# Performance work log

Measured on AMD Instinct MI355X. Metric: run time of the kernel, lower is better.

## Reference

```python
import jax, jax.numpy as jnp
import numpy as np

B = 16384
NUM_DENSE = 13
NUM_SPARSE = 26
VOCAB = 100000
EMB = 64
MLP_DIMS = [512, 256, 64]
TOP_OUT = 256
TRIU_I, TRIU_J = np.triu_indices(NUM_SPARSE, k=1)  # 325 pairs


def setup_inputs() -> dict:
    key = jax.random.key(0)
    ks = jax.random.split(key, 12)
    inp = {}
    inp["dense_features"] = jax.random.normal(ks[0], (B, NUM_DENSE), dtype=jnp.float32)
    inp["sparse_features"] = jax.random.randint(ks[1], (B, NUM_SPARSE), 0, VOCAB, dtype=jnp.int64)
    # embedding tables, all same shape -> stacked [F, V, D]
    inp["tables"] = jax.random.normal(ks[2], (NUM_SPARSE, VOCAB, EMB), dtype=jnp.float32) * 0.01
    # bottom (dense) MLP: 13 -> 512 -> 256 -> 64, weights stored [in, out]
    dims = [NUM_DENSE] + MLP_DIMS
    for li in range(3):
        fan_in = dims[li]
        inp[f"W{li}"] = jax.random.normal(ks[3 + li], (dims[li], dims[li + 1]), dtype=jnp.float32) / np.sqrt(fan_in)
        inp[f"b{li}"] = jnp.zeros((dims[li + 1],), dtype=jnp.float32)
    # top MLP: (64 + 325) -> 256
    top_in = MLP_DIMS[-1] + NUM_SPARSE * (NUM_SPARSE - 1) // 2
    inp["Wt"] = jax.random.normal(ks[6], (top_in, TOP_OUT), dtype=jnp.float32) / np.sqrt(top_in)
    inp["bt"] = jnp.zeros((TOP_OUT,), dtype=jnp.float32)
    return inp


def reference(dense_features, sparse_features, tables, W0, b0, W1, b1, W2, b2, Wt, bt):
    # bottom MLP with ReLU after every layer (as in the torch Sequential)
    x = jax.nn.relu(dense_features @ W0 + b0)
    x = jax.nn.relu(x @ W1 + b1)
    dense_out = jax.nn.relu(x @ W2 + b2)  # [B, 64]

    # embedding gather: table f indexed by sparse_features[:, f] -> [B, F, D]
    emb = jax.vmap(lambda t, idx: t[idx], in_axes=(0, 1), out_axes=1)(tables, sparse_features)

    # pairwise dot interaction, upper triangle (i < j) -> [B, 325]
    gram = jnp.einsum('bid,bjd->bij', emb, emb)
    interact = gram[:, TRIU_I, TRIU_J]

    features = jnp.concatenate([dense_out, interact], axis=1)  # [B, 389]
    return features @ Wt + bt  # [B, 256]
```

## Files before the change

### kernel.cpp

```cpp
#include <hip/hip_runtime.h>
#include <hip/hip_bf16.h>


#define BATCH   16384
#define NSPARSE 26
#define VOCAB   100000
#define EMB     64
#define KTOP    416
#define KREAL   389
#define SPB     32
#define ASTR    424
#define X1STR   520
#define X2STR   264

typedef __attribute__((ext_vector_type(8)))  short bf16x8;
typedef __attribute__((ext_vector_type(4)))  short s16x4;
typedef __attribute__((ext_vector_type(4)))  float f32x4;
typedef __attribute__((ext_vector_type(16))) float f32x16;

__device__ inline void gload_lds16(const void* g, void* l) {
    __builtin_amdgcn_global_load_lds(
        (const __attribute__((address_space(1))) void*)g,
        (__attribute__((address_space(3))) void*)l, 16, 0, 0);
}

__device__ inline short f2bf(float x) {
    __hip_bfloat16 h = __float2bfloat16(x);
    return *reinterpret_cast<short*>(&h);
}

__global__ __launch_bounds__(256)
void prep_weights(const float* __restrict__ W0, const float* __restrict__ W1,
                  const float* __restrict__ W2, const float* __restrict__ Wt,
                  short* __restrict__ W0t, short* __restrict__ W1t,
                  short* __restrict__ W2t, short* __restrict__ Wtt)
{
    __shared__ float tile[32][36];
    int b = blockIdx.x, t = threadIdx.x;
    const float* src; short* dst; int K, N, Kpad, k0, n0;
    if (b < 16)        {              src = W0; dst = W0t; K = 13;  N = 512; Kpad = 32;  k0 = 0;           n0 = b * 32; }
    else if (b < 144)  { int i = b - 16;  src = W1; dst = W1t; K = 512; N = 256; Kpad = 512; k0 = (i >> 3) * 32; n0 = (i & 7) * 32; }
    else if (b < 160)  { int i = b - 144; src = W2; dst = W2t; K = 256; N = 64;  Kpad = 256; k0 = (i >> 1) * 32; n0 = (i & 1) * 32; }
    else               { int i = b - 160; src = Wt; dst = Wtt; K = 389; N = 256; Kpad = 416; k0 = (i >> 3) * 32; n0 = (i & 7) * 32; }

    int r = t >> 3, c4 = (t & 7) * 4;
    int gr = k0 + r;
    float4 v = make_float4(0.f, 0.f, 0.f, 0.f);
    if (gr < K) v = *(const float4*)(src + (size_t)gr * N + n0 + c4);
    tile[r][c4 + 0] = v.x; tile[r][c4 + 1] = v.y;
    tile[r][c4 + 2] = v.z; tile[r][c4 + 3] = v.w;
    __syncthreads();
    s16x4 o;
    #pragma unroll
    for (int j = 0; j < 4; ++j) o[j] = f2bf(tile[c4 + j][r]);
    *(s16x4*)&dst[(size_t)(n0 + r) * Kpad + k0 + c4] = o;
}

__global__ __launch_bounds__(256, 2)
void fused_all(const int* __restrict__ sparse, const float* __restrict__ tables,
               const float* __restrict__ D,
               const short* __restrict__ W0t, const float* __restrict__ b0,
               const short* __restrict__ W1t, const float* __restrict__ b1,
               const short* __restrict__ W2t, const float* __restrict__ b2,
               const short* __restrict__ Wtt, const float* __restrict__ bt,
               float* __restrict__ out)
{
    __shared__ __align__(16) char smem[78848];
    short* As  = (short*)(smem);
    short* X1s = (short*)(smem + 27136);
    short* X2s = (short*)(smem + 27136);
    short* Bst = (short*)(smem + 60416);
    short* Ds  = (short*)(smem + 76800);

    int tid = threadIdx.x;
    int w = tid >> 6, lane = tid & 63;
    int lr = lane & 15, lg = lane >> 4;
    int wr = w >> 1, wc = w & 1;
    int swz = (lg ^ (lr & 3)) * 8;
    int sbase = blockIdx.x * SPB;

    for (int x = tid; x < SPB * 13; x += 256) {
        int r = x / 13, k = x - r * 13;
        Ds[r * 32 + k] = f2bf(D[(size_t)sbase * 13 + x]);
    }
    for (int x = tid; x < SPB * 19; x += 256) {
        int r = x / 19, k = 13 + (x - r * 19);
        Ds[r * 32 + k] = 0;
    }
    for (int x = tid; x < SPB * 27; x += 256) {
        int r = x / 27, c = x - r * 27;
        As[r * ASTR + KREAL + c] = 0;
    }
    __syncthreads();

    auto gram_phase = [&]() {
        int row = lane & 31, half = lane >> 5;
        int srow = (row < NSPARSE) ? row : 0;
        int idxv[8];
        #pragma unroll
        for (int li = 0; li < 8; ++li)
            idxv[li] = sparse[(sbase + w * 8 + li) * NSPARSE + srow];

        f32x4 Ca[4], Cb[4], Na[4], Nb[4];
        {
            const float* rp = tables + ((long)srow * VOCAB + idxv[0]) * EMB + half * 8;
            #pragma unroll
            for (int t = 0; t < 4; ++t) {
                Ca[t] = *(const f32x4*)(rp + t * 16);
                Cb[t] = *(const f32x4*)(rp + t * 16 + 4);
            }
        }
        #pragma unroll
        for (int li = 0; li < 8; ++li) {
            if (li < 7) {
                const float* rp = tables + ((long)srow * VOCAB + idxv[li + 1]) * EMB + half * 8;
                #pragma unroll
                for (int t = 0; t < 4; ++t) {
                    Na[t] = *(const f32x4*)(rp + t * 16);
                    Nb[t] = *(const f32x4*)(rp + t * 16 + 4);
                }
            }
            f32x16 acc = {};
            #pragma unroll
            for (int t = 0; t < 4; ++t) {
                bf16x8 f;
                #pragma unroll
                for (int j = 0; j < 4; ++j) f[j] = f2bf(Ca[t][j]);
                #pragma unroll
                for (int j = 0; j < 4; ++j) f[4 + j] = f2bf(Cb[t][j]);
                acc = __builtin_amdgcn_mfma_f32_32x32x16_bf16(f, f, acc, 0, 0, 0);
            }
            int c = row;
            if (c < NSPARSE) {
                #pragma unroll
                for (int reg = 0; reg < 16; ++reg) {
                    int r = (reg & 3) + 8 * (reg >> 2) + 4 * half;
                    if (r < c) {
                        int p = r * (2 * NSPARSE - r - 1) / 2 + (c - r - 1);
                        As[(w * 8 + li) * ASTR + 64 + p] = f2bf(acc[reg]);
                    }
                }
            }
            #pragma unroll
            for (int t = 0; t < 4; ++t) { Ca[t] = Na[t]; Cb[t] = Nb[t]; }
        }
    };

    auto mlp_phase = [&]() {
        {
            bf16x8 a = *(const bf16x8*)&Ds[(wr * 16 + lr) * 32 + lg * 8];
            f32x4 acc[16] = {};
            #pragma unroll
            for (int ni = 0; ni < 16; ++ni) {
                bf16x8 b = *(const bf16x8*)(W0t + (size_t)(wc * 256 + ni * 16 + lr) * 32 + lg * 8);
                acc[ni] = __builtin_amdgcn_mfma_f32_16x16x32_bf16(a, b, acc[ni], 0, 0, 0);
            }
            #pragma unroll
            for (int ni = 0; ni < 16; ++ni) {
                int col = wc * 256 + ni * 16 + lr;
                float bv = b0[col];
                #pragma unroll
                for (int j = 0; j < 4; ++j) {
                    int r = wr * 16 + lg * 4 + j;
                    X1s[r * X1STR + col] = f2bf(fmaxf(acc[ni][j] + bv, 0.f));
                }
            }
        }
        {
            f32x4 acc[8] = {};
            for (int k0 = 0; k0 < 512; k0 += 32) {
                #pragma unroll
                for (int rd = 0; rd < 4; ++rd) {
                    int slot = rd * 256 + tid;
                    int n = slot >> 2, kc = slot & 3;
                    gload_lds16(W1t + (size_t)n * 512 + k0 + (kc ^ (n & 3)) * 8, &Bst[slot * 8]);
                }
                __syncthreads();
                bf16x8 a = *(const bf16x8*)&X1s[(wr * 16 + lr) * X1STR + k0 + lg * 8];
                #pragma unroll
                for (int ni = 0; ni < 8; ++ni) {
                    int n = wc * 128 + ni * 16 + lr;
                    bf16x8 b = *(const bf16x8*)&Bst[n * 32 + swz];
                    acc[ni] = __builtin_amdgcn_mfma_f32_16x16x32_bf16(a, b, acc[ni], 0, 0, 0);
                }
                __syncthreads();
            }
            #pragma unroll
            for (int ni = 0; ni < 8; ++ni) {
                int col = wc * 128 + ni * 16 + lr;
                float bv = b1[col];
                #pragma unroll
                for (int j = 0; j < 4; ++j) {
                    int r = wr * 16 + lg * 4 + j;
                    X2s[r * X2STR + col] = f2bf(fmaxf(acc[ni][j] + bv, 0.f));
                }
            }
        }
        {
            f32x4 acc[2] = {};
            for (int k0 = 0; k0 < 256; k0 += 32) {
                {
                    int n = tid >> 2, kc = tid & 3;
                    gload_lds16(W2t + (size_t)n * 256 + k0 + (kc ^ (n & 3)) * 8, &Bst[tid * 8]);
                }
                __syncthreads();
                bf16x8 a = *(const bf16x8*)&X2s[(wr * 16 + lr) * X2STR + k0 + lg * 8];
                #pragma unroll
                for (int ni = 0; ni < 2; ++ni) {
                    int n = wc * 32 + ni * 16 + lr;
                    bf16x8 b = *(const bf16x8*)&Bst[n * 32 + swz];
                    acc[ni] = __builtin_amdgcn_mfma_f32_16x16x32_bf16(a, b, acc[ni], 0, 0, 0);
                }
                __syncthreads();
            }
            #pragma unroll
            for (int ni = 0; ni < 2; ++ni) {
                int col = wc * 32 + ni * 16 + lr;
                float bv = b2[col];
                #pragma unroll
                for (int j = 0; j < 4; ++j) {
                    int r = wr * 16 + lg * 4 + j;
                    As[r * ASTR + col] = f2bf(fmaxf(acc[ni][j] + bv, 0.f));
                }
            }
        }
    };

    if ((blockIdx.x >> 8) & 1) { mlp_phase(); gram_phase(); }
    else                       { gram_phase(); mlp_phase(); }

    {
        f32x4 acc[8] = {};
        for (int k0 = 0; k0 < KTOP; k0 += 32) {
            #pragma unroll
            for (int rd = 0; rd < 4; ++rd) {
                int slot = rd * 256 + tid;
                int n = slot >> 2, kc = slot & 3;
                gload_lds16(Wtt + (size_t)n * KTOP + k0 + (kc ^ (n & 3)) * 8, &Bst[slot * 8]);
            }
            __syncthreads();
            bf16x8 a = *(const bf16x8*)&As[(wr * 16 + lr) * ASTR + k0 + lg * 8];
            #pragma unroll
            for (int ni = 0; ni < 8; ++ni) {
                int n = wc * 128 + ni * 16 + lr;
                bf16x8 b = *(const bf16x8*)&Bst[n * 32 + swz];
                acc[ni] = __builtin_amdgcn_mfma_f32_16x16x32_bf16(a, b, acc[ni], 0, 0, 0);
            }
            __syncthreads();
        }
        #pragma unroll
        for (int ni = 0; ni < 8; ++ni) {
            int col = wc * 128 + ni * 16 + lr;
            float bv = bt[col];
            #pragma unroll
            for (int j = 0; j < 4; ++j) {
                int r = wr * 16 + lg * 4 + j;
                out[(size_t)(sbase + r) * 256 + col] = acc[ni][j] + bv;
            }
        }
    }
}

extern "C" void kernel_launch(void* const* d_in, const int* in_sizes, int n_in,
                              void* d_out, int out_size, void* d_ws, size_t ws_size,
                              hipStream_t stream)
{
    const float* dense  = (const float*)d_in[0];
    const int*   sparse = (const int*)  d_in[1];
    const float* tables = (const float*)d_in[2];
    const float* W0     = (const float*)d_in[3];
    const float* b0     = (const float*)d_in[4];
    const float* W1     = (const float*)d_in[5];
    const float* b1     = (const float*)d_in[6];
    const float* W2     = (const float*)d_in[7];
    const float* b2     = (const float*)d_in[8];
    const float* Wt     = (const float*)d_in[9];
    const float* bt     = (const float*)d_in[10];
    float* out = (float*)d_out;

    char* ws = (char*)d_ws;
    short* W0t = (short*)(ws);
    short* W1t = (short*)(ws + 32768);
    short* W2t = (short*)(ws + 294912);
    short* Wtt = (short*)(ws + 327680);

    prep_weights<<<264, 256, 0, stream>>>(W0, W1, W2, Wt, W0t, W1t, W2t, Wtt);

    fused_all<<<BATCH / SPB, 256, 0, stream>>>(sparse, tables, dense,
                                               W0t, b0, W1t, b1, W2t, b2,
                                               Wtt, bt, out);
}
```

Before: 52.03 us.

## Halve samples per block and double-buffer weight staging in LDS

Each block now handles 16 samples instead of 32, so the grid doubles. Each of the 4 waves now owns a column slice of the 16-row tile, where before waves were split into row and column halves. The weight tiles for the W1, W2 and top GEMMs are now double-buffered in LDS: the next K-slice is prefetched with global_load_lds while MFMAs run on the current one, which removes one barrier per iteration. In exchange, each block reloads all the weights for only half as many rows, doubling total weight traffic from L2. The separate X1 and X2 buffers also change the LDS layout.

```diff
diff --git a/kernel.cpp b/kernel.cpp
--- a/kernel.cpp
+++ b/kernel.cpp
@@ -8,7 +8,7 @@
 #define EMB     64
 #define KTOP    416
 #define KREAL   389
-#define SPB     32
+#define SPB     16
 #define ASTR    424
 #define X1STR   520
 #define X2STR   264
@@ -65,19 +65,35 @@
                const short* __restrict__ Wtt, const float* __restrict__ bt,
                float* __restrict__ out)
 {
-    __shared__ __align__(16) char smem[78848];
-    short* As  = (short*)(smem);
-    short* X1s = (short*)(smem + 27136);
-    short* X2s = (short*)(smem + 27136);
-    short* Bst = (short*)(smem + 60416);
-    short* Ds  = (short*)(smem + 76800);
+    __shared__ __align__(16) char smem[72448];
+    short* Ds   = (short*)(smem);
+    short* As   = (short*)(smem + 1024);
+    short* X1s  = (short*)(smem + 14592);
+    short* X2s  = (short*)(smem + 31232);
+    short* Bst0 = (short*)(smem + 39680);
+    short* Bst1 = (short*)(smem + 56064);
+    short* Bst[2] = {Bst0, Bst1};
 
     int tid = threadIdx.x;
     int w = tid >> 6, lane = tid & 63;
     int lr = lane & 15, lg = lane >> 4;
-    int wr = w >> 1, wc = w & 1;
     int swz = (lg ^ (lr & 3)) * 8;
     int sbase = blockIdx.x * SPB;
+
+    auto stage256 = [&](short* dstBuf, const short* W, int ldw, int k0) {
+        #pragma unroll
+        for (int rd = 0; rd < 4; ++rd) {
+            int slot = rd * 256 + tid;
+            int n = slot >> 2, kc = slot & 3;
+            gload_lds16(W + (size_t)n * ldw + k0 + (kc ^ (n & 3)) * 8,
+                        dstBuf + slot * 8);
+        }
+    };
+    auto stage64 = [&](short* dstBuf, const short* W, int ldw, int k0) {
+        int n = tid >> 2, kc = tid & 3;
+        gload_lds16(W + (size_t)n * ldw + k0 + (kc ^ (n & 3)) * 8,
+                    dstBuf + tid * 8);
+    };
 
     for (int x = tid; x < SPB * 13; x += 256) {
         int r = x / 13, k = x - r * 13;
@@ -96,10 +112,10 @@
     auto gram_phase = [&]() {
         int row = lane & 31, half = lane >> 5;
         int srow = (row < NSPARSE) ? row : 0;
-        int idxv[8];
-        #pragma unroll
-        for (int li = 0; li < 8; ++li)
-            idxv[li] = sparse[(sbase + w * 8 + li) * NSPARSE + srow];
+        int idxv[4];
+        #pragma unroll
+        for (int li = 0; li < 4; ++li)
+            idxv[li] = sparse[(sbase + w * 4 + li) * NSPARSE + srow];
 
         f32x4 Ca[4], Cb[4], Na[4], Nb[4];
         {
@@ -111,8 +127,8 @@
             }
         }
         #pragma unroll
-        for (int li = 0; li < 8; ++li) {
-            if (li < 7) {
+        for (int li = 0; li < 4; ++li) {
+            if (li < 3) {
                 const float* rp = tables + ((long)srow * VOCAB + idxv[li + 1]) * EMB + half * 8;
                 #pragma unroll
                 for (int t = 0; t < 4; ++t) {
@@ -137,7 +153,7 @@
                     int r = (reg & 3) + 8 * (reg >> 2) + 4 * half;
                     if (r < c) {
                         int p = r * (2 * NSPARSE - r - 1) / 2 + (c - r - 1);
-                        As[(w * 8 + li) * ASTR + 64 + p] = f2bf(acc[reg]);
+                        As[(w * 4 + li) * ASTR + 64 + p] = f2bf(acc[reg]);
                     }
                 }
             }
@@ -148,113 +164,94 @@
 
     auto mlp_phase = [&]() {
         {
-            bf16x8 a = *(const bf16x8*)&Ds[(wr * 16 + lr) * 32 + lg * 8];
-            f32x4 acc[16] = {};
-            #pragma unroll
-            for (int ni = 0; ni < 16; ++ni) {
-                bf16x8 b = *(const bf16x8*)(W0t + (size_t)(wc * 256 + ni * 16 + lr) * 32 + lg * 8);
+            bf16x8 a = *(const bf16x8*)&Ds[lr * 32 + lg * 8];
+            f32x4 acc[8] = {};
+            #pragma unroll
+            for (int ni = 0; ni < 8; ++ni) {
+                bf16x8 b = *(const bf16x8*)(W0t + (size_t)(w * 128 + ni * 16 + lr) * 32 + lg * 8);
                 acc[ni] = __builtin_amdgcn_mfma_f32_16x16x32_bf16(a, b, acc[ni], 0, 0, 0);
             }
             #pragma unroll
-            for (int ni = 0; ni < 16; ++ni) {
-                int col = wc * 256 + ni * 16 + lr;
+            for (int ni = 0; ni < 8; ++ni) {
+                int col = w * 128 + ni * 16 + lr;
                 float bv = b0[col];
                 #pragma unroll
-                for (int j = 0; j < 4; ++j) {
-                    int r = wr * 16 + lg * 4 + j;
-                    X1s[r * X1STR + col] = f2bf(fmaxf(acc[ni][j] + bv, 0.f));
-                }
-            }
-        }
-        {
-            f32x4 acc[8] = {};
-            for (int k0 = 0; k0 < 512; k0 += 32) {
-                #pragma unroll
-                for (int rd = 0; rd < 4; ++rd) {
-                    int slot = rd * 256 + tid;
-                    int n = slot >> 2, kc = slot & 3;
-                    gload_lds16(W1t + (size_t)n * 512 + k0 + (kc ^ (n & 3)) * 8, &Bst[slot * 8]);
-                }
-                __syncthreads();
-                bf16x8 a = *(const bf16x8*)&X1s[(wr * 16 + lr) * X1STR + k0 + lg * 8];
-                #pragma unroll
-                for (int ni = 0; ni < 8; ++ni) {
-                    int n = wc * 128 + ni * 16 + lr;
-                    bf16x8 b = *(const bf16x8*)&Bst[n * 32 + swz];
+                for (int j = 0; j < 4; ++j)
+                    X1s[(lg * 4 + j) * X1STR + col] = f2bf(fmaxf(acc[ni][j] + bv, 0.f));
+            }
+        }
+        stage256(Bst[0], W1t, 512, 0);
+        __syncthreads();
+        {
+            f32x4 acc[4] = {};
+            int s = 0;
+            for (int k0 = 0; k0 < 512; k0 += 32, s ^= 1) {
+                if (k0 + 32 < 512) stage256(Bst[s ^ 1], W1t, 512, k0 + 32);
+                bf16x8 a = *(const bf16x8*)&X1s[lr * X1STR + k0 + lg * 8];
+                #pragma unroll
+                for (int ni = 0; ni < 4; ++ni) {
+                    int n = w * 64 + ni * 16 + lr;
+                    bf16x8 b = *(const bf16x8*)&Bst[s][n * 32 + swz];
                     acc[ni] = __builtin_amdgcn_mfma_f32_16x16x32_bf16(a, b, acc[ni], 0, 0, 0);
                 }
                 __syncthreads();
             }
             #pragma unroll
-            for (int ni = 0; ni < 8; ++ni) {
-                int col = wc * 128 + ni * 16 + lr;
+            for (int ni = 0; ni < 4; ++ni) {
+                int col = w * 64 + ni * 16 + lr;
                 float bv = b1[col];
                 #pragma unroll
-                for (int j = 0; j < 4; ++j) {
-                    int r = wr * 16 + lg * 4 + j;
-                    X2s[r * X2STR + col] = f2bf(fmaxf(acc[ni][j] + bv, 0.f));
-                }
-            }
-        }
-        {
-            f32x4 acc[2] = {};
-            for (int k0 = 0; k0 < 256; k0 += 32) {
-                {
-                    int n = tid >> 2, kc = tid & 3;
-                    gload_lds16(W2t + (size_t)n * 256 + k0 + (kc ^ (n & 3)) * 8, &Bst[tid * 8]);
-                }
+                for (int j = 0; j < 4; ++j)
+                    X2s[(lg * 4 + j) * X2STR + col] = f2bf(fmaxf(acc[ni][j] + bv, 0.f));
+            }
+        }
+        stage64(Bst[0], W2t, 256, 0);
+        __syncthreads();
+        {
+            f32x4 acc = {};
+            int s = 0;
+            for (int k0 = 0; k0 < 256; k0 += 32, s ^= 1) {
+                if (k0 + 32 < 256) stage64(Bst[s ^ 1], W2t, 256, k0 + 32);
+                bf16x8 a = *(const bf16x8*)&X2s[lr * X2STR + k0 + lg * 8];
+                int n = w * 16 + lr;
+                bf16x8 b = *(const bf16x8*)&Bst[s][n * 32 + swz];
+                acc = __builtin_amdgcn_mfma_f32_16x16x32_bf16(a, b, acc, 0, 0, 0);
                 __syncthreads();
-                bf16x8 a = *(const bf16x8*)&X2s[(wr * 16 + lr) * X2STR + k0 + lg * 8];
-                #pragma unroll
-                for (int ni = 0; ni < 2; ++ni) {
-                    int n = wc * 32 + ni * 16 + lr;
-                    bf16x8 b = *(const bf16x8*)&Bst[n * 32 + swz];
-                    acc[ni] = __builtin_amdgcn_mfma_f32_16x16x32_bf16(a, b, acc[ni], 0, 0, 0);
-                }
-                __syncthreads();
-            }
-            #pragma unroll
-            for (int ni = 0; ni < 2; ++ni) {
-                int col = wc * 32 + ni * 16 + lr;
-                float bv = b2[col];
-                #pragma unroll
-                for (int j = 0; j < 4; ++j) {
-                    int r = wr * 16 + lg * 4 + j;
-                    As[r * ASTR + col] = f2bf(fmaxf(acc[ni][j] + bv, 0.f));
-                }
-            }
-        }
-    };
-
-    if ((blockIdx.x >> 8) & 1) { mlp_phase(); gram_phase(); }
+            }
+            int col = w * 16 + lr;
+            float bv = b2[col];
+            #pragma unroll
+            for (int j = 0; j < 4; ++j)
+                As[(lg * 4 + j) * ASTR + col] = f2bf(fmaxf(acc[j] + bv, 0.f));
+        }
+    };
+
+    if ((blockIdx.x >> 9) & 1) { mlp_phase(); gram_phase(); }
     else                       { gram_phase(); mlp_phase(); }
 
+    stage256(Bst[0], Wtt, KTOP, 0);
+    __syncthreads();
     {
-        f32x4 acc[8] = {};
-        for (int k0 = 0; k0 < KTOP; k0 += 32) {
-            #pragma unroll
-            for (int rd = 0; rd < 4; ++rd) {
-                int slot = rd * 256 + tid;
-                int n = slot >> 2, kc = slot & 3;
-                gload_lds16(Wtt + (size_t)n * KTOP + k0 + (kc ^ (n & 3)) * 8, &Bst[slot * 8]);
+        f32x4 acc[4] = {};
+        int s = 0;
+        for (int k0 = 0; k0 < KTOP; k0 += 32, s ^= 1) {
+            if (k0 + 32 < KTOP) stage256(Bst[s ^ 1], Wtt, KTOP, k0 + 32);
+            bf16x8 a = *(const bf16x8*)&As[lr * ASTR + k0 + lg * 8];
+            #pragma unroll
+            for (int ni = 0; ni < 4; ++ni) {
+                int n = w * 64 + ni * 16 + lr;
+                bf16x8 b = *(const bf16x8*)&Bst[s][n * 32 + swz];
+                acc[ni] = __builtin_amdgcn_mfma_f32_16x16x32_bf16(a, b, acc[ni], 0, 0, 0);
             }
             __syncthreads();
-            bf16x8 a = *(const bf16x8*)&As[(wr * 16 + lr) * ASTR + k0 + lg * 8];
-            #pragma unroll
-            for (int ni = 0; ni < 8; ++ni) {
-                int n = wc * 128 + ni * 16 + lr;
-                bf16x8 b = *(const bf16x8*)&Bst[n * 32 + swz];
-                acc[ni] = __builtin_amdgcn_mfma_f32_16x16x32_bf16(a, b, acc[ni], 0, 0, 0);
-            }
-            __syncthreads();
-        }
-        #pragma unroll
-        for (int ni = 0; ni < 8; ++ni) {
-            int col = wc * 128 + ni * 16 + lr;
+        }
+        #pragma unroll
+        for (int ni = 0; ni < 4; ++ni) {
+            int col = w * 64 + ni * 16 + lr;
             float bv = bt[col];
             #pragma unroll
             for (int j = 0; j < 4; ++j) {
-                int r = wr * 16 + lg * 4 + j;
+                int r = lg * 4 + j;
                 out[(size_t)(sbase + r) * 256 + col] = acc[ni][j] + bv;
             }
         }
```

After: 65.30 us. 25.5% more time.

## Stage embedding gathers through LDS via async global_load_lds with swizzle

Applied to the files above, without the earlier changes.

The embedding gather changes from per-lane register loads with software prefetch to a cooperative async global-to-LDS copy. Each of 8 groups loads the 26 rows for 4 samples into a swizzled LDS buffer, and the MFMA gram step then reads from LDS. Indices are staged into LDS once per block. The change also drops the alternating MLP/gram phase order across blocks and adds barriers between the MLP stages. In exchange it adds two block-wide barriers per group and loses the cross-block mixing of memory-heavy and compute-heavy phases.

```diff
diff --git a/kernel.cpp b/kernel.cpp
--- a/kernel.cpp
+++ b/kernel.cpp
@@ -66,11 +66,13 @@
                float* __restrict__ out)
 {
     __shared__ __align__(16) char smem[78848];
-    short* As  = (short*)(smem);
-    short* X1s = (short*)(smem + 27136);
-    short* X2s = (short*)(smem + 27136);
-    short* Bst = (short*)(smem + 60416);
-    short* Ds  = (short*)(smem + 76800);
+    short* As   = (short*)(smem);
+    short* X1s  = (short*)(smem + 27136);
+    short* X2s  = (short*)(smem + 27136);
+    float* gbuf = (float*)(smem + 27136);
+    int*  idxb  = (int*)  (smem + 53760);
+    short* Bst  = (short*)(smem + 60416);
+    short* Ds   = (short*)(smem + 76800);
 
     int tid = threadIdx.x;
     int w = tid >> 6, lane = tid & 63;
@@ -79,6 +81,8 @@
     int swz = (lg ^ (lr & 3)) * 8;
     int sbase = blockIdx.x * SPB;
 
+    for (int x = tid; x < SPB * NSPARSE; x += 256)
+        idxb[x] = sparse[(size_t)sbase * NSPARSE + x];
     for (int x = tid; x < SPB * 13; x += 256) {
         int r = x / 13, k = x - r * 13;
         Ds[r * 32 + k] = f2bf(D[(size_t)sbase * 13 + x]);
@@ -93,41 +97,39 @@
     }
     __syncthreads();
 
-    auto gram_phase = [&]() {
+    {
         int row = lane & 31, half = lane >> 5;
         int srow = (row < NSPARSE) ? row : 0;
-        int idxv[8];
-        #pragma unroll
-        for (int li = 0; li < 8; ++li)
-            idxv[li] = sparse[(sbase + w * 8 + li) * NSPARSE + srow];
-
-        f32x4 Ca[4], Cb[4], Na[4], Nb[4];
-        {
-            const float* rp = tables + ((long)srow * VOCAB + idxv[0]) * EMB + half * 8;
+        int x7 = srow & 7;
+        const float* myrow = gbuf + srow * 64;
+
+        for (int g = 0; g < 8; ++g) {
+            #pragma unroll
+            for (int it = 0; it < 7; ++it) {
+                int c = it * 256 + tid;
+                if (c < 1664) {
+                    int sl = c / 416, rem = c - sl * 416;
+                    int r = rem >> 4, s = rem & 15;
+                    int idx = idxb[(g * 4 + sl) * NSPARSE + r];
+                    const float* src = tables + ((long)r * VOCAB + idx) * EMB
+                                       + (s ^ (r & 7)) * 4;
+                    gload_lds16(src, (char*)gbuf + c * 16);
+                }
+            }
+            __syncthreads();
+
+            const float* sp = myrow + w * 1664;
+            f32x16 acc = {};
             #pragma unroll
             for (int t = 0; t < 4; ++t) {
-                Ca[t] = *(const f32x4*)(rp + t * 16);
-                Cb[t] = *(const f32x4*)(rp + t * 16 + 4);
-            }
-        }
-        #pragma unroll
-        for (int li = 0; li < 8; ++li) {
-            if (li < 7) {
-                const float* rp = tables + ((long)srow * VOCAB + idxv[li + 1]) * EMB + half * 8;
-                #pragma unroll
-                for (int t = 0; t < 4; ++t) {
-                    Na[t] = *(const f32x4*)(rp + t * 16);
-                    Nb[t] = *(const f32x4*)(rp + t * 16 + 4);
-                }
-            }
-            f32x16 acc = {};
-            #pragma unroll
-            for (int t = 0; t < 4; ++t) {
+                int s0 = half * 2 + t * 4;
+                f32x4 ca = *(const f32x4*)(sp + (s0 ^ x7) * 4);
+                f32x4 cb = *(const f32x4*)(sp + ((s0 + 1) ^ x7) * 4);
                 bf16x8 f;
                 #pragma unroll
-                for (int j = 0; j < 4; ++j) f[j] = f2bf(Ca[t][j]);
-                #pragma unroll
-                for (int j = 0; j < 4; ++j) f[4 + j] = f2bf(Cb[t][j]);
+                for (int j = 0; j < 4; ++j) f[j] = f2bf(ca[j]);
+                #pragma unroll
+                for (int j = 0; j < 4; ++j) f[4 + j] = f2bf(cb[j]);
                 acc = __builtin_amdgcn_mfma_f32_32x32x16_bf16(f, f, acc, 0, 0, 0);
             }
             int c = row;
@@ -137,16 +139,15 @@
                     int r = (reg & 3) + 8 * (reg >> 2) + 4 * half;
                     if (r < c) {
                         int p = r * (2 * NSPARSE - r - 1) / 2 + (c - r - 1);
-                        As[(w * 8 + li) * ASTR + 64 + p] = f2bf(acc[reg]);
+                        As[(g * 4 + w) * ASTR + 64 + p] = f2bf(acc[reg]);
                     }
                 }
             }
-            #pragma unroll
-            for (int t = 0; t < 4; ++t) { Ca[t] = Na[t]; Cb[t] = Nb[t]; }
-        }
-    };
-
-    auto mlp_phase = [&]() {
+            __syncthreads();
+        }
+    }
+
+    {
         {
             bf16x8 a = *(const bf16x8*)&Ds[(wr * 16 + lr) * 32 + lg * 8];
             f32x4 acc[16] = {};
@@ -166,6 +167,7 @@
                 }
             }
         }
+        __syncthreads();
         {
             f32x4 acc[8] = {};
             for (int k0 = 0; k0 < 512; k0 += 32) {
@@ -196,6 +198,7 @@
                 }
             }
         }
+        __syncthreads();
         {
             f32x4 acc[2] = {};
             for (int k0 = 0; k0 < 256; k0 += 32) {
@@ -224,10 +227,8 @@
                 }
             }
         }
-    };
-
-    if ((blockIdx.x >> 8) & 1) { mlp_phase(); gram_phase(); }
-    else                       { gram_phase(); mlp_phase(); }
+        __syncthreads();
+    }
 
     {
         f32x4 acc[8] = {};
```

After: 54.46 us. +4.7%, slower.

## Double samples per block with 512 threads and double-buffered weight staging

Applied to the files above, without the earlier changes.

Each block now handles 64 samples with 8 waves instead of 32 samples with 4 waves. Every staged weight tile is reused across twice as many rows, which roughly halves global weight traffic per sample. Weight tiles are now double-buffered in LDS, so the load of the next k-slice overlaps the MFMAs and one barrier per iteration is removed. The mlp/gram phase alternation across blocks is dropped. LDS use grows to about 154KB, which allows one block per CU and lowers occupancy and latency hiding for the embedding gathers.

```diff
diff --git a/kernel.cpp b/kernel.cpp
--- a/kernel.cpp
+++ b/kernel.cpp
@@ -8,7 +8,7 @@
 #define EMB     64
 #define KTOP    416
 #define KREAL   389
-#define SPB     32
+#define SPB     64
 #define ASTR    424
 #define X1STR   520
 #define X2STR   264
@@ -56,7 +56,7 @@
     *(s16x4*)&dst[(size_t)(n0 + r) * Kpad + k0 + c4] = o;
 }
 
-__global__ __launch_bounds__(256, 2)
+__global__ __launch_bounds__(512, 1)
 void fused_all(const int* __restrict__ sparse, const float* __restrict__ tables,
                const float* __restrict__ D,
                const short* __restrict__ W0t, const float* __restrict__ b0,
@@ -65,35 +65,54 @@
                const short* __restrict__ Wtt, const float* __restrict__ bt,
                float* __restrict__ out)
 {
-    __shared__ __align__(16) char smem[78848];
-    short* As  = (short*)(smem);
-    short* X1s = (short*)(smem + 27136);
-    short* X2s = (short*)(smem + 27136);
-    short* Bst = (short*)(smem + 60416);
-    short* Ds  = (short*)(smem + 76800);
+    __shared__ __align__(16) char smem[157696];
+    short* Ds   = (short*)(smem);
+    short* As   = (short*)(smem + 4096);
+    short* X1s  = (short*)(smem + 58368);
+    short* X2s  = (short*)(smem + 58368);
+    short* Bst0 = (short*)(smem + 124928);
+    short* Bst1 = (short*)(smem + 141312);
+    short* bufs[2] = {Bst0, Bst1};
 
     int tid = threadIdx.x;
     int w = tid >> 6, lane = tid & 63;
     int lr = lane & 15, lg = lane >> 4;
-    int wr = w >> 1, wc = w & 1;
+    int wr = w >> 2, wc = w & 3;
     int swz = (lg ^ (lr & 3)) * 8;
     int sbase = blockIdx.x * SPB;
 
-    for (int x = tid; x < SPB * 13; x += 256) {
+    auto stage256 = [&](short* dstBuf, const short* W, int ldw, int k0) {
+        #pragma unroll
+        for (int rd = 0; rd < 2; ++rd) {
+            int slot = rd * 512 + tid;
+            int n = slot >> 2, kc = slot & 3;
+            gload_lds16(W + (size_t)n * ldw + k0 + (kc ^ (n & 3)) * 8,
+                        dstBuf + slot * 8);
+        }
+    };
+    auto stage64 = [&](short* dstBuf, const short* W, int ldw, int k0) {
+        if (tid < 256) {
+            int n = tid >> 2, kc = tid & 3;
+            gload_lds16(W + (size_t)n * ldw + k0 + (kc ^ (n & 3)) * 8,
+                        dstBuf + tid * 8);
+        }
+    };
+
+    for (int x = tid; x < SPB * 13; x += 512) {
         int r = x / 13, k = x - r * 13;
         Ds[r * 32 + k] = f2bf(D[(size_t)sbase * 13 + x]);
     }
-    for (int x = tid; x < SPB * 19; x += 256) {
+    for (int x = tid; x < SPB * 19; x += 512) {
         int r = x / 19, k = 13 + (x - r * 19);
         Ds[r * 32 + k] = 0;
     }
-    for (int x = tid; x < SPB * 27; x += 256) {
+    for (int x = tid; x < SPB * 27; x += 512) {
         int r = x / 27, c = x - r * 27;
         As[r * ASTR + KREAL + c] = 0;
     }
     __syncthreads();
 
-    auto gram_phase = [&]() {
+    {
         int row = lane & 31, half = lane >> 5;
         int srow = (row < NSPARSE) ? row : 0;
         int idxv[8];
@@ -144,119 +163,119 @@
             #pragma unroll
             for (int t = 0; t < 4; ++t) { Ca[t] = Na[t]; Cb[t] = Nb[t]; }
         }
-    };
-
-    auto mlp_phase = [&]() {
-        {
-            bf16x8 a = *(const bf16x8*)&Ds[(wr * 16 + lr) * 32 + lg * 8];
-            f32x4 acc[16] = {};
-            #pragma unroll
-            for (int ni = 0; ni < 16; ++ni) {
-                bf16x8 b = *(const bf16x8*)(W0t + (size_t)(wc * 256 + ni * 16 + lr) * 32 + lg * 8);
-                acc[ni] = __builtin_amdgcn_mfma_f32_16x16x32_bf16(a, b, acc[ni], 0, 0, 0);
-            }
-            #pragma unroll
-            for (int ni = 0; ni < 16; ++ni) {
-                int col = wc * 256 + ni * 16 + lr;
-                float bv = b0[col];
-                #pragma unroll
-                for (int j = 0; j < 4; ++j) {
-                    int r = wr * 16 + lg * 4 + j;
-                    X1s[r * X1STR + col] = f2bf(fmaxf(acc[ni][j] + bv, 0.f));
-                }
-            }
-        }
-        {
-            f32x4 acc[8] = {};
-            for (int k0 = 0; k0 < 512; k0 += 32) {
-                #pragma unroll
-                for (int rd = 0; rd < 4; ++rd) {
-                    int slot = rd * 256 + tid;
-                    int n = slot >> 2, kc = slot & 3;
-                    gload_lds16(W1t + (size_t)n * 512 + k0 + (kc ^ (n & 3)) * 8, &Bst[slot * 8]);
-                }
-                __syncthreads();
-                bf16x8 a = *(const bf16x8*)&X1s[(wr * 16 + lr) * X1STR + k0 + lg * 8];
-                #pragma unroll
-                for (int ni = 0; ni < 8; ++ni) {
-                    int n = wc * 128 + ni * 16 + lr;
-                    bf16x8 b = *(const bf16x8*)&Bst[n * 32 + swz];
-                    acc[ni] = __builtin_amdgcn_mfma_f32_16x16x32_bf16(a, b, acc[ni], 0, 0, 0);
-                }
-                __syncthreads();
-            }
-            #pragma unroll
-            for (int ni = 0; ni < 8; ++ni) {
-                int col = wc * 128 + ni * 16 + lr;
-                float bv = b1[col];
-                #pragma unroll
-                for (int j = 0; j < 4; ++j) {
-                    int r = wr * 16 + lg * 4 + j;
-                    X2s[r * X2STR + col] = f2bf(fmaxf(acc[ni][j] + bv, 0.f));
-                }
-            }
-        }
-        {
-            f32x4 acc[2] = {};
-            for (int k0 = 0; k0 < 256; k0 += 32) {
-                {
-                    int n = tid >> 2, kc = tid & 3;
-                    gload_lds16(W2t + (size_t)n * 256 + k0 + (kc ^ (n & 3)) * 8, &Bst[tid * 8]);
-                }
-                __syncthreads();
-                bf16x8 a = *(const bf16x8*)&X2s[(wr * 16 + lr) * X2STR + k0 + lg * 8];
-                #pragma unroll
-                for (int ni = 0; ni < 2; ++ni) {
-                    int n = wc * 32 + ni * 16 + lr;
-                    bf16x8 b = *(const bf16x8*)&Bst[n * 32 + swz];
-                    acc[ni] = __builtin_amdgcn_mfma_f32_16x16x32_bf16(a, b, acc[ni], 0, 0, 0);
-                }
-                __syncthreads();
-            }
-            #pragma unroll
-            for (int ni = 0; ni < 2; ++ni) {
-                int col = wc * 32 + ni * 16 + lr;
-                float bv = b2[col];
-                #pragma unroll
-                for (int j = 0; j < 4; ++j) {
-                    int r = wr * 16 + lg * 4 + j;
-                    As[r * ASTR + col] = f2bf(fmaxf(acc[ni][j] + bv, 0.f));
-                }
-            }
-        }
-    };
-
-    if ((blockIdx.x >> 8) & 1) { mlp_phase(); gram_phase(); }
-    else                       { gram_phase(); mlp_phase(); }
-
-    {
-        f32x4 acc[8] = {};
-        for (int k0 = 0; k0 < KTOP; k0 += 32) {
-            #pragma unroll
-            for (int rd = 0; rd < 4; ++rd) {
-                int slot = rd * 256 + tid;
-                int n = slot >> 2, kc = slot & 3;
-                gload_lds16(Wtt + (size_t)n * KTOP + k0 + (kc ^ (n & 3)) * 8, &Bst[slot * 8]);
-            }
-            __syncthreads();
-            bf16x8 a = *(const bf16x8*)&As[(wr * 16 + lr) * ASTR + k0 + lg * 8];
-            #pragma unroll
-            for (int ni = 0; ni < 8; ++ni) {
-                int n = wc * 128 + ni * 16 + lr;
-                bf16x8 b = *(const bf16x8*)&Bst[n * 32 + swz];
-                acc[ni] = __builtin_amdgcn_mfma_f32_16x16x32_bf16(a, b, acc[ni], 0, 0, 0);
-            }
-            __syncthreads();
+    }
+
+    {
+        bf16x8 a0 = *(const bf16x8*)&Ds[(wr * 32 + lr) * 32 + lg * 8];
+        bf16x8 a1 = *(const bf16x8*)&Ds[(wr * 32 + 16 + lr) * 32 + lg * 8];
+        f32x4 acc[2][8] = {};
+        #pragma unroll
+        for (int ni = 0; ni < 8; ++ni) {
+            bf16x8 b = *(const bf16x8*)(W0t + (size_t)(wc * 128 + ni * 16 + lr) * 32 + lg * 8);
+            acc[0][ni] = __builtin_amdgcn_mfma_f32_16x16x32_bf16(a0, b, acc[0][ni], 0, 0, 0);
+            acc[1][ni] = __builtin_amdgcn_mfma_f32_16x16x32_bf16(a1, b, acc[1][ni], 0, 0, 0);
         }
         #pragma unroll
         for (int ni = 0; ni < 8; ++ni) {
             int col = wc * 128 + ni * 16 + lr;
+            float bv = b0[col];
+            #pragma unroll
+            for (int mi = 0; mi < 2; ++mi)
+                #pragma unroll
+                for (int j = 0; j < 4; ++j) {
+                    int r = wr * 32 + mi * 16 + lg * 4 + j;
+                    X1s[r * X1STR + col] = f2bf(fmaxf(acc[mi][ni][j] + bv, 0.f));
+                }
+        }
+    }
+
+    stage256(bufs[0], W1t, 512, 0);
+    __syncthreads();
+    {
+        f32x4 acc[2][4] = {};
+        int s = 0;
+        for (int k0 = 0; k0 < 512; k0 += 32, s ^= 1) {
+            if (k0 + 32 < 512) stage256(bufs[s ^ 1], W1t, 512, k0 + 32);
+            bf16x8 a0 = *(const bf16x8*)&X1s[(wr * 32 + lr) * X1STR + k0 + lg * 8];
+            bf16x8 a1 = *(const bf16x8*)&X1s[(wr * 32 + 16 + lr) * X1STR + k0 + lg * 8];
+            #pragma unroll
+            for (int ni = 0; ni < 4; ++ni) {
+                int n = wc * 64 + ni * 16 + lr;
+                bf16x8 b = *(const bf16x8*)&bufs[s][n * 32 + swz];
+                acc[0][ni] = __builtin_amdgcn_mfma_f32_16x16x32_bf16(a0, b, acc[0][ni], 0, 0, 0);
+                acc[1][ni] = __builtin_amdgcn_mfma_f32_16x16x32_bf16(a1, b, acc[1][ni], 0, 0, 0);
+            }
+            __syncthreads();
+        }
+        #pragma unroll
+        for (int ni = 0; ni < 4; ++ni) {
+            int col = wc * 64 + ni * 16 + lr;
+            float bv = b1[col];
+            #pragma unroll
+            for (int mi = 0; mi < 2; ++mi)
+                #pragma unroll
+                for (int j = 0; j < 4; ++j) {
+                    int r = wr * 32 + mi * 16 + lg * 4 + j;
+                    X2s[r * X2STR + col] = f2bf(fmaxf(acc[mi][ni][j] + bv, 0.f));
+                }
+        }
+    }
+
+    stage64(bufs[0], W2t, 256, 0);
+    __syncthreads();
+    {
+        f32x4 acc[2] = {};
+        int s = 0;
+        for (int k0 = 0; k0 < 256; k0 += 32, s ^= 1) {
+            if (k0 + 32 < 256) stage64(bufs[s ^ 1], W2t, 256, k0 + 32);
+            bf16x8 a0 = *(const bf16x8*)&X2s[(wr * 32 + lr) * X2STR + k0 + lg * 8];
+            bf16x8 a1 = *(const bf16x8*)&X2s[(wr * 32 + 16 + lr) * X2STR + k0 + lg * 8];
+            int n = wc * 16 + lr;
+            bf16x8 b = *(const bf16x8*)&bufs[s][n * 32 + swz];
+            acc[0] = __builtin_amdgcn_mfma_f32_16x16x32_bf16(a0, b, acc[0], 0, 0, 0);
+            acc[1] = __builtin_amdgcn_mfma_f32_16x16x32_bf16(a1, b, acc[1], 0, 0, 0);
+            __syncthreads();
+        }
+        int col = wc * 16 + lr;
+        float bv = b2[col];
+        #pragma unroll
+        for (int mi = 0; mi < 2; ++mi)
+            #pragma unroll
+            for (int j = 0; j < 4; ++j) {
+                int r = wr * 32 + mi * 16 + lg * 4 + j;
+                As[r * ASTR + col] = f2bf(fmaxf(acc[mi][j] + bv, 0.f));
+            }
+    }
+
+    stage256(bufs[0], Wtt, KTOP, 0);
+    __syncthreads();
+    {
+        f32x4 acc[2][4] = {};
+        int s = 0;
+        for (int k0 = 0; k0 < KTOP; k0 += 32, s ^= 1) {
+            if (k0 + 32 < KTOP) stage256(bufs[s ^ 1], Wtt, KTOP, k0 + 32);
+            bf16x8 a0 = *(const bf16x8*)&As[(wr * 32 + lr) * ASTR + k0 + lg * 8];
+            bf16x8 a1 = *(const bf16x8*)&As[(wr * 32 + 16 + lr) * ASTR + k0 + lg * 8];
+            #pragma unroll
+            for (int ni = 0; ni < 4; ++ni) {
+                int n = wc * 64 + ni * 16 + lr;
+                bf16x8 b = *(const bf16x8*)&bufs[s][n * 32 + swz];
+                acc[0][ni] = __builtin_amdgcn_mfma_f32_16x16x32_bf16(a0, b, acc[0][ni], 0, 0, 0);
+                acc[1][ni] = __builtin_amdgcn_mfma_f32_16x16x32_bf16(a1, b, acc[1][ni], 0, 0, 0);
+            }
+            __syncthreads();
+        }
+        #pragma unroll
+        for (int ni = 0; ni < 4; ++ni) {
+            int col = wc * 64 + ni * 16 + lr;
             float bv = bt[col];
             #pragma unroll
-            for (int j = 0; j < 4; ++j) {
-                int r = wr * 16 + lg * 4 + j;
-                out[(size_t)(sbase + r) * 256 + col] = acc[ni][j] + bv;
-            }
+            for (int mi = 0; mi < 2; ++mi)
+                #pragma unroll
+                for (int j = 0; j < 4; ++j) {
+                    int r = wr * 32 + mi * 16 + lg * 4 + j;
+                    out[(size_t)(sbase + r) * 256 + col] = acc[mi][ni][j] + bv;
+                }
         }
     }
 }
@@ -286,7 +305,7 @@
 
     prep_weights<<<264, 256, 0, stream>>>(W0, W1, W2, Wt, W0t, W1t, W2t, Wtt);
 
-    fused_all<<<BATCH / SPB, 256, 0, stream>>>(sparse, tables, dense,
+    fused_all<<<BATCH / SPB, 512, 0, stream>>>(sparse, tables, dense,
                                                W0t, b0, W1t, b1, W2t, b2,
                                                Wtt, bt, out);
 }
```

Measured after the change: 48.13 us. 7.5% less time.
